# Kernel optimization log

Hardware: AMD Instinct MI355X
Metric: run time of the kernel (lower is better)

Reference implementation:

```python
import jax, jax.numpy as jnp
import numpy as np

BINS = 256
LO = -4.0
HI = 4.0


def setup_inputs() -> dict:
    key = jax.random.key(0)
    k1, _ = jax.random.split(key)
    x = jax.random.normal(k1, (67108864,), dtype=jnp.float32)
    out = jnp.zeros((BINS,), dtype=jnp.float32)
    return {"x": x, "out": out}


def _histc(x):
    # torch.histc semantics: bins equal-width over [LO, HI]; values == HI go in
    # the last bin; values outside [LO, HI] are ignored.
    scale = jnp.float32(BINS / (HI - LO))
    idx = jnp.floor((x - jnp.float32(LO)) * scale).astype(jnp.int32)
    idx = jnp.minimum(idx, BINS - 1)  # x == HI -> last bin
    valid = (x >= LO) & (x <= HI)
    idx = jnp.where(valid, idx, BINS)  # route out-of-range to a discard bin
    hist = jax.ops.segment_sum(jnp.ones_like(x), idx, num_segments=BINS + 1)
    return hist[:BINS]


def reference(x, out):
    h = _histc(x)
    return (h, h)
```

## Files before the change

### kernel.cpp

```cpp
#include <hip/hip_runtime.h>

#define BINS 256
#define NLO (-4.0f)
#define NHI (4.0f)
#define SCALE 32.0f

constexpr int TPB = 256;

__device__ __forceinline__ void bin_one(float v, unsigned* h) {
    float t = (v - NLO) * SCALE;
    int b = (int)floorf(t);
    b = b > (BINS - 1) ? (BINS - 1) : b;
    if (v >= NLO && v <= NHI) {
        atomicAdd(&h[b], 1u);
    }
}

__global__ __launch_bounds__(TPB, 4) void hist_partial(
        const float4* __restrict__ x4, int n4,
        const float* __restrict__ x, int n,
        unsigned* __restrict__ partials) {
    __shared__ unsigned lds[4 * BINS];
    const int tid = threadIdx.x;

    #pragma unroll
    for (int i = tid; i < 4 * BINS; i += TPB) lds[i] = 0;
    __syncthreads();

    unsigned* h = lds + (tid >> 6) * BINS;

    const int stride = gridDim.x * TPB;
    int i = blockIdx.x * TPB + tid;

    for (; i + 3 * stride < n4; i += 4 * stride) {
        float4 a = x4[i];
        float4 b = x4[i + stride];
        float4 c = x4[i + 2 * stride];
        float4 d = x4[i + 3 * stride];
        bin_one(a.x, h); bin_one(a.y, h); bin_one(a.z, h); bin_one(a.w, h);
        bin_one(b.x, h); bin_one(b.y, h); bin_one(b.z, h); bin_one(b.w, h);
        bin_one(c.x, h); bin_one(c.y, h); bin_one(c.z, h); bin_one(c.w, h);
        bin_one(d.x, h); bin_one(d.y, h); bin_one(d.z, h); bin_one(d.w, h);
    }
    for (; i < n4; i += stride) {
        float4 a = x4[i];
        bin_one(a.x, h); bin_one(a.y, h); bin_one(a.z, h); bin_one(a.w, h);
    }
    if (blockIdx.x == 0) {
        int tail = n - n4 * 4;
        if (tid < tail) bin_one(x[n4 * 4 + tid], h);
    }

    __syncthreads();

    unsigned total = lds[tid] + lds[BINS + tid] + lds[2 * BINS + tid] + lds[3 * BINS + tid];
    partials[(size_t)blockIdx.x * BINS + tid] = total;
}

__global__ void hist_reduce(const unsigned* __restrict__ partials, int P,
                            float* __restrict__ out) {
    const int bin = blockIdx.x;
    const int lane = threadIdx.x;
    unsigned s = 0;
    for (int p = lane; p < P; p += 64)
        s += partials[(size_t)p * BINS + bin];
    #pragma unroll
    for (int off = 32; off > 0; off >>= 1)
        s += __shfl_down(s, off);
    if (lane == 0) {
        float f = (float)s;
        out[bin] = f;
        out[BINS + bin] = f;
    }
}

extern "C" void kernel_launch(void* const* d_in, const int* in_sizes, int n_in,
                              void* d_out, int out_size, void* d_ws, size_t ws_size,
                              hipStream_t stream) {
    const float* x = (const float*)d_in[0];
    const int n = in_sizes[0];
    const int n4 = n / 4;

    int P = (int)(ws_size / (BINS * sizeof(unsigned)));
    if (P > 1024) P = 1024;
    if (P < 1) P = 1;

    unsigned* partials = (unsigned*)d_ws;
    float* out = (float*)d_out;

    hist_partial<<<P, TPB, 0, stream>>>((const float4*)x, n4, x, n, partials);
    hist_reduce<<<BINS, 64, 0, stream>>>(partials, P, out);
}
```

Before: 356.8 us.

## Fuse histogram reduction via global float atomics, branchless binning, nontemporal loads

Replaces the partials workspace and separate reduce kernel with direct float atomicAdd of each block's LDS histogram into the output, preceded by a tiny zeroing kernel. Binning becomes branchless by routing out-of-range values to a discard slot, with the per-wave LDS stride padded to 257. The main loop uses nontemporal loads and 8-deep unrolling, and the grid grows to 2048 blocks. The aim is to cut the reduce launch and partials traffic and keep more loads in flight. The cost is more global atomics, and out-of-range values now still issue an LDS atomic.

```diff
diff --git a/kernel.cpp b/kernel.cpp
--- a/kernel.cpp
+++ b/kernel.cpp
@@ -1,49 +1,55 @@
 #include <hip/hip_runtime.h>
 
 #define BINS 256
-#define NLO (-4.0f)
-#define NHI (4.0f)
-#define SCALE 32.0f
+#define HSTRIDE 257
+constexpr int TPB  = 256;
+constexpr int GRID = 2048;
 
-constexpr int TPB = 256;
+typedef float f32x4 __attribute__((ext_vector_type(4)));
 
 __device__ __forceinline__ void bin_one(float v, unsigned* h) {
-    float t = (v - NLO) * SCALE;
+    float t = (v + 4.0f) * 32.0f;
     int b = (int)floorf(t);
     b = b > (BINS - 1) ? (BINS - 1) : b;
-    if (v >= NLO && v <= NHI) {
-        atomicAdd(&h[b], 1u);
-    }
+    bool valid = (v >= -4.0f) && (v <= 4.0f);
+    int idx = valid ? b : BINS;
+    atomicAdd(&h[idx], 1u);
 }
 
-__global__ __launch_bounds__(TPB, 4) void hist_partial(
-        const float4* __restrict__ x4, int n4,
+__global__ void zero_out(float* __restrict__ out) {
+    int i = blockIdx.x * blockDim.x + threadIdx.x;
+    if (i < 2 * BINS) out[i] = 0.0f;
+}
+
+__global__ __launch_bounds__(TPB) void hist_main(
+        const f32x4* __restrict__ x4, int n4,
         const float* __restrict__ x, int n,
-        unsigned* __restrict__ partials) {
-    __shared__ unsigned lds[4 * BINS];
+        float* __restrict__ out) {
+    __shared__ unsigned lds[4 * HSTRIDE];
     const int tid = threadIdx.x;
 
     #pragma unroll
-    for (int i = tid; i < 4 * BINS; i += TPB) lds[i] = 0;
+    for (int i = tid; i < 4 * HSTRIDE; i += TPB) lds[i] = 0;
     __syncthreads();
 
-    unsigned* h = lds + (tid >> 6) * BINS;
+    unsigned* h = lds + (tid >> 6) * HSTRIDE;
 
     const int stride = gridDim.x * TPB;
     int i = blockIdx.x * TPB + tid;
 
-    for (; i + 3 * stride < n4; i += 4 * stride) {
-        float4 a = x4[i];
-        float4 b = x4[i + stride];
-        float4 c = x4[i + 2 * stride];
-        float4 d = x4[i + 3 * stride];
-        bin_one(a.x, h); bin_one(a.y, h); bin_one(a.z, h); bin_one(a.w, h);
-        bin_one(b.x, h); bin_one(b.y, h); bin_one(b.z, h); bin_one(b.w, h);
-        bin_one(c.x, h); bin_one(c.y, h); bin_one(c.z, h); bin_one(c.w, h);
-        bin_one(d.x, h); bin_one(d.y, h); bin_one(d.z, h); bin_one(d.w, h);
+    for (; i + 7 * stride < n4; i += 8 * stride) {
+        f32x4 v[8];
+        #pragma unroll
+        for (int j = 0; j < 8; ++j)
+            v[j] = __builtin_nontemporal_load(&x4[i + j * stride]);
+        #pragma unroll
+        for (int j = 0; j < 8; ++j) {
+            bin_one(v[j].x, h); bin_one(v[j].y, h);
+            bin_one(v[j].z, h); bin_one(v[j].w, h);
+        }
     }
     for (; i < n4; i += stride) {
-        float4 a = x4[i];
+        f32x4 a = __builtin_nontemporal_load(&x4[i]);
         bin_one(a.x, h); bin_one(a.y, h); bin_one(a.z, h); bin_one(a.w, h);
     }
     if (blockIdx.x == 0) {
@@ -53,25 +59,11 @@
 
     __syncthreads();
 
-    unsigned total = lds[tid] + lds[BINS + tid] + lds[2 * BINS + tid] + lds[3 * BINS + tid];
-    partials[(size_t)blockIdx.x * BINS + tid] = total;
-}
-
-__global__ void hist_reduce(const unsigned* __restrict__ partials, int P,
-                            float* __restrict__ out) {
-    const int bin = blockIdx.x;
-    const int lane = threadIdx.x;
-    unsigned s = 0;
-    for (int p = lane; p < P; p += 64)
-        s += partials[(size_t)p * BINS + bin];
-    #pragma unroll
-    for (int off = 32; off > 0; off >>= 1)
-        s += __shfl_down(s, off);
-    if (lane == 0) {
-        float f = (float)s;
-        out[bin] = f;
-        out[BINS + bin] = f;
-    }
+    unsigned total = lds[tid] + lds[HSTRIDE + tid]
+                   + lds[2 * HSTRIDE + tid] + lds[3 * HSTRIDE + tid];
+    float f = (float)total;
+    atomicAdd(&out[tid], f);
+    atomicAdd(&out[BINS + tid], f);
 }
 
 extern "C" void kernel_launch(void* const* d_in, const int* in_sizes, int n_in,
@@ -80,14 +72,8 @@
     const float* x = (const float*)d_in[0];
     const int n = in_sizes[0];
     const int n4 = n / 4;
-
-    int P = (int)(ws_size / (BINS * sizeof(unsigned)));
-    if (P > 1024) P = 1024;
-    if (P < 1) P = 1;
-
-    unsigned* partials = (unsigned*)d_ws;
     float* out = (float*)d_out;
 
-    hist_partial<<<P, TPB, 0, stream>>>((const float4*)x, n4, x, n, partials);
-    hist_reduce<<<BINS, 64, 0, stream>>>(partials, P, out);
+    zero_out<<<1, 2 * BINS, 0, stream>>>(out);
+    hist_main<<<GRID, TPB, 0, stream>>>((const f32x4*)x, n4, x, n, out);
 }
```

New measurement: 355.1 us. No clear change (-0.5%).
